# Kernel optimization log

Hardware: AMD Instinct MI355X
Metric: run time of the kernel (lower is better)

Reference implementation:

```python
import jax, jax.numpy as jnp
import numpy as np

B, N, D, H = 32, 4096, 768, 384

def setup_inputs() -> dict:
    key = jax.random.key(0)
    k1, k2, k3 = jax.random.split(key, 3)
    patch_tokens = jax.random.normal(k1, (B, N, D), dtype=jnp.float32)
    # score head params (kaiming-like scale)
    w1 = jax.random.normal(k2, (D, H), dtype=jnp.float32) * (2.0 / H) ** 0.5
    b1 = jnp.zeros((H,), dtype=jnp.float32)
    w2 = jax.random.normal(k3, (H,), dtype=jnp.float32) * (2.0 / 1) ** 0.5
    b2 = jnp.zeros((), dtype=jnp.float32)
    return {"patch_tokens": patch_tokens, "w1": w1, "b1": b1, "w2": w2, "b2": b2,
            "keep_ratio_pct": 50}

def reference(patch_tokens, w1, b1, w2, b2, keep_ratio_pct):
    # score head: Linear -> GELU (erf variant, torch default) -> Linear(->1)
    h = jax.nn.gelu(jnp.einsum('bnd,dh->bnh', patch_tokens, w1) + b1, approximate=False)
    patch_logits = jnp.einsum('bnh,h->bn', h, w2) + b2                 # [B, N]
    foreground_scores = jax.nn.sigmoid(patch_logits)                    # [B, N]

    patch_count = patch_tokens.shape[1]
    keep_count = max(1, int(patch_count * keep_ratio_pct / 100))
    keep_count = min(keep_count, patch_count)

    if keep_count == patch_count:
        keep_mask = jnp.ones_like(foreground_scores)
    else:
        topk_scores, _ = jax.lax.top_k(foreground_scores, keep_count)   # [B, k], sorted desc
        keep_threshold = jax.lax.stop_gradient(topk_scores[:, -1:])     # [B, 1]
        keep_mask = (foreground_scores >= keep_threshold).astype(foreground_scores.dtype)

    filtered_scores = foreground_scores * keep_mask
    filtered_weights = filtered_scores / (jnp.sum(filtered_scores, axis=1, keepdims=True) + 1e-12)
    filtered_feat = jnp.einsum('bn,bnd->bd', filtered_weights, patch_tokens)  # [B, D]
    return (filtered_feat, filtered_weights, foreground_scores, keep_mask)
```

## Files before the change

kernel.cpp:

```cpp
#include <hip/hip_runtime.h>
#include <math.h>

#define BB 32
#define NN 4096
#define DD 768
#define HH 384
#define NCH 8

typedef _Float16 half8 __attribute__((ext_vector_type(8)));
typedef float f32x4 __attribute__((ext_vector_type(4)));

__global__ __launch_bounds__(64) void fapf_prep_w(
    const float* __restrict__ w1, short* __restrict__ whf, short* __restrict__ wlf)
{
    const int cf = blockIdx.x;
    const int kg = blockIdx.y;
    const int l  = threadIdx.x;
    const int c  = cf * 16 + (l & 15);
    const int kb = kg * 32 + (l >> 4) * 8;

    short hs[8], ls[8];
#pragma unroll
    for (int i = 0; i < 8; i++) {
        float v = w1[(size_t)(kb + i) * HH + c];
        _Float16 hi = (_Float16)v;
        _Float16 lo = (_Float16)(v - (float)hi);
        hs[i] = *(short*)&hi;
        ls[i] = *(short*)&lo;
    }
    size_t base = ((size_t)(kg * 24 + cf) * 64 + l) * 8;
#pragma unroll
    for (int i = 0; i < 8; i++) { whf[base + i] = hs[i]; wlf[base + i] = ls[i]; }
}

__global__ __launch_bounds__(256)
__attribute__((amdgpu_waves_per_eu(3)))
void fapf_scores_mfma(
    const float* __restrict__ x, const short* __restrict__ whf,
    const short* __restrict__ wlf, const float* __restrict__ b1,
    const float* __restrict__ w2, const float* __restrict__ b2,
    float* __restrict__ scores)
{
    __shared__ __align__(16) short xh[2][32 * 64];
    __shared__ __align__(16) short xl[2][32 * 64];
    __shared__ float part[32][4];

    const int tid = threadIdx.x;
    const int l   = tid & 63;
    const int cw  = tid >> 6;
    const int t0  = blockIdx.x * 32;

    f32x4 acc[2][6];
#pragma unroll
    for (int fr = 0; fr < 2; fr++)
#pragma unroll
        for (int cf = 0; cf < 6; cf++) acc[fr][cf] = (f32x4){0.f, 0.f, 0.f, 0.f};

    const half8* whp = (const half8*)whf + (size_t)(cw * 6) * 64 + l;
    const half8* wlp = (const half8*)wlf + (size_t)(cw * 6) * 64 + l;

    float4 xv[2];

#define LOADX(ch)                                                            \
    {                                                                        \
        _Pragma("unroll")                                                    \
        for (int it = 0; it < 2; it++) {                                     \
            int id = it * 256 + tid;                                         \
            xv[it] = *(const float4*)&x[(size_t)(t0 + (id >> 4)) * DD        \
                                        + (ch) * 64 + (id & 15) * 4];        \
        }                                                                    \
    }

#define SPLITWRITE(buf)                                                      \
    {                                                                        \
        _Pragma("unroll")                                                    \
        for (int it = 0; it < 2; it++) {                                     \
            int id = it * 256 + tid;                                         \
            int row = id >> 4, seg = id & 15;                                \
            union { short s[4]; uint2 u; } ph, pl;                           \
            float vv[4] = {xv[it].x, xv[it].y, xv[it].z, xv[it].w};          \
            _Pragma("unroll")                                                \
            for (int i = 0; i < 4; i++) {                                    \
                _Float16 hi = (_Float16)vv[i];                               \
                _Float16 lo = (_Float16)(vv[i] - (float)hi);                 \
                ph.s[i] = *(short*)&hi;                                      \
                pl.s[i] = *(short*)&lo;                                      \
            }                                                                \
            int idx = (row * 64 + seg * 4) ^ ((row & 7) << 3);               \
            *(uint2*)&xh[buf][idx] = ph.u;                                   \
            *(uint2*)&xl[buf][idx] = pl.u;                                   \
        }                                                                    \
    }

#define LOADB(dst, ptr, kg)                                                  \
    {                                                                        \
        _Pragma("unroll")                                                    \
        for (int cf = 0; cf < 6; cf++)                                       \
            dst[cf] = (ptr)[(size_t)(kg) * 1536 + (size_t)cf * 64];          \
    }

    LOADX(0);
    SPLITWRITE(0);
    half8 bA[6], bB[6];
    LOADB(bA, whp, 0);
    __syncthreads();
    LOADX(1);

    for (int c = 0; c < 12; c++) {
        const int cur = c & 1;

#pragma unroll
        for (int ks = 0; ks < 2; ks++) {
            const int kg = c * 2 + ks;

            half8 ah[2], al[2];
#pragma unroll
            for (int fr = 0; fr < 2; fr++) {
                int row = fr * 16 + (l & 15);
                int idx = (row * 64 + ks * 32 + (l >> 4) * 8) ^ ((row & 7) << 3);
                ah[fr] = *(const half8*)&xh[cur][idx];
                al[fr] = *(const half8*)&xl[cur][idx];
            }

            LOADB(bB, wlp, kg);

            __builtin_amdgcn_s_setprio(1);
#pragma unroll
            for (int fr = 0; fr < 2; fr++)
#pragma unroll
                for (int cf = 0; cf < 6; cf++)
                    acc[fr][cf] = __builtin_amdgcn_mfma_f32_16x16x32_f16(
                        ah[fr], bA[cf], acc[fr][cf], 0, 0, 0);
#pragma unroll
            for (int fr = 0; fr < 2; fr++)
#pragma unroll
                for (int cf = 0; cf < 6; cf++)
                    acc[fr][cf] = __builtin_amdgcn_mfma_f32_16x16x32_f16(
                        al[fr], bA[cf], acc[fr][cf], 0, 0, 0);
            __builtin_amdgcn_s_setprio(0);

            if (kg < 23) LOADB(bA, whp, kg + 1);

            __builtin_amdgcn_s_setprio(1);
#pragma unroll
            for (int fr = 0; fr < 2; fr++)
#pragma unroll
                for (int cf = 0; cf < 6; cf++)
                    acc[fr][cf] = __builtin_amdgcn_mfma_f32_16x16x32_f16(
                        ah[fr], bB[cf], acc[fr][cf], 0, 0, 0);
            __builtin_amdgcn_s_setprio(0);
        }

        if (c < 11) {
            SPLITWRITE(cur ^ 1);
            __syncthreads();
            if (c < 10) LOADX(c + 2);
        }
    }

    float b1v[6], w2v[6];
#pragma unroll
    for (int cf = 0; cf < 6; cf++) {
        int col = cw * 96 + cf * 16 + (l & 15);
        b1v[cf] = b1[col];
        w2v[cf] = w2[col];
    }
    float p[2][4];
#pragma unroll
    for (int fr = 0; fr < 2; fr++)
#pragma unroll
        for (int j = 0; j < 4; j++) p[fr][j] = 0.f;
#pragma unroll
    for (int fr = 0; fr < 2; fr++)
#pragma unroll
        for (int cf = 0; cf < 6; cf++)
#pragma unroll
            for (int j = 0; j < 4; j++) {
                float hh = acc[fr][cf][j] + b1v[cf];
                float g  = 0.5f * hh * (1.f + erff(hh * 0.70710678118654752f));
                p[fr][j] = fmaf(g, w2v[cf], p[fr][j]);
            }
#pragma unroll
    for (int m = 8; m >= 1; m >>= 1)
#pragma unroll
        for (int fr = 0; fr < 2; fr++)
#pragma unroll
            for (int j = 0; j < 4; j++)
                p[fr][j] += __shfl_xor(p[fr][j], m, 64);

    if ((l & 15) == 0) {
#pragma unroll
        for (int fr = 0; fr < 2; fr++)
#pragma unroll
            for (int j = 0; j < 4; j++) {
                int row = fr * 16 + (l >> 4) * 4 + j;
                part[row][cw] = p[fr][j];
            }
    }
    __syncthreads();
    if (tid < 32) {
        float lg = part[tid][0] + part[tid][1] + part[tid][2] + part[tid][3] + b2[0];
        scores[t0 + tid] = 1.f / (1.f + expf(-lg));
    }
#undef LOADX
#undef SPLITWRITE
#undef LOADB
}

__global__ __launch_bounds__(1024) void fapf_select_kernel(
    const float* __restrict__ scores, const int* __restrict__ pct_p,
    float* __restrict__ weights, float* __restrict__ mask,
    float* __restrict__ feat, int* __restrict__ kidx,
    float* __restrict__ kw, int* __restrict__ kcnt)
{
    __shared__ float s[NN];
    __shared__ float red[1024];
    __shared__ int scnt;
    const int b = blockIdx.x, tid = threadIdx.x;

    if (tid == 0) scnt = 0;
    for (int i = tid; i < DD; i += 1024) feat[b * DD + i] = 0.f;
    for (int i = tid; i < NN; i += 1024) s[i] = scores[b * NN + i];
    __syncthreads();

    for (int k = 2; k <= NN; k <<= 1) {
        for (int j = k >> 1; j > 0; j >>= 1) {
            for (int i = tid; i < NN; i += 1024) {
                int ixj = i ^ j;
                if (ixj > i) {
                    bool up = ((i & k) == 0);
                    float a = s[i], c = s[ixj];
                    if (up ? (a > c) : (a < c)) { s[i] = c; s[ixj] = a; }
                }
            }
            __syncthreads();
        }
    }

    int pct = pct_p[0];
    long long kcl = (long long)NN * pct / 100;
    int kc = (int)kcl;
    if (kc < 1) kc = 1;
    if (kc > NN) kc = NN;
    float thr = s[NN - kc];

    float local = 0.f;
    for (int i = tid; i < NN; i += 1024) {
        float v = scores[b * NN + i];
        if (v >= thr) local += v;
    }
    red[tid] = local;
    __syncthreads();
    for (int step = 512; step > 0; step >>= 1) {
        if (tid < step) red[tid] += red[tid + step];
        __syncthreads();
    }
    float inv = 1.f / (red[0] + 1e-12f);
    const int lane = tid & 63;
    for (int i = tid; i < NN; i += 1024) {
        float v = scores[b * NN + i];
        bool keep = (v >= thr);
        float m = keep ? 1.f : 0.f;
        weights[b * NN + i] = v * m * inv;
        mask[b * NN + i]    = m;
        if (kidx) {
            unsigned long long bal = __ballot(keep);
            int base = 0;
            if (lane == 0) base = atomicAdd(&scnt, __popcll(bal));
            base = __shfl(base, 0, 64);
            if (keep) {
                int off = __popcll(bal & ((1ULL << lane) - 1ULL));
                kidx[b * NN + base + off] = i;
                kw[b * NN + base + off]   = v * inv;
            }
        }
    }
    if (kidx) {
        __syncthreads();
        if (tid == 0) kcnt[b] = scnt;
    }
}

__global__ __launch_bounds__(256) void fapf_feat_compact(
    const float* __restrict__ x, const int* __restrict__ kidx,
    const float* __restrict__ kw, const int* __restrict__ kcnt,
    float* __restrict__ feat)
{
    const int b  = blockIdx.y;
    const int d0 = blockIdx.x * 64;
    const int ch = blockIdx.z;
    const int dl = threadIdx.x & 63;
    const int ng = threadIdx.x >> 6;

    const int cnt = kcnt[b];
    int per = (cnt + NCH - 1) / NCH;
    int j0 = ch * per; if (j0 > cnt) j0 = cnt;
    int j1 = j0 + per; if (j1 > cnt) j1 = cnt;
    int len = j1 - j0;
    int per_w = (len + 3) >> 2;
    int s = j0 + ng * per_w;
    int e = s + per_w; if (e > j1) e = j1;

    const float* xb  = x + (size_t)b * NN * DD + d0 + dl;
    const int*   ib  = kidx + b * NN;
    const float* wbp = kw + b * NN;

    float a[8];
#pragma unroll
    for (int u = 0; u < 8; u++) a[u] = 0.f;

    int j = s;
    for (; j + 8 <= e; j += 8) {
        int   idx[8];
        float ww[8];
#pragma unroll
        for (int u = 0; u < 8; u++) { idx[u] = ib[j + u]; ww[u] = wbp[j + u]; }
#pragma unroll
        for (int u = 0; u < 8; u++)
            a[u] = fmaf(ww[u], xb[(size_t)idx[u] * DD], a[u]);
    }
    for (; j < e; j++)
        a[0] = fmaf(wbp[j], xb[(size_t)ib[j] * DD], a[0]);

    float acc = ((a[0] + a[1]) + (a[2] + a[3])) + ((a[4] + a[5]) + (a[6] + a[7]));

    __shared__ float red[4][64];
    red[ng][dl] = acc;
    __syncthreads();
    if (threadIdx.x < 64) {
        float v = (red[0][dl] + red[1][dl]) + (red[2][dl] + red[3][dl]);
        atomicAdd(&feat[b * DD + d0 + dl], v);
    }
}

__global__ __launch_bounds__(256) void fapf_feat_dense(
    const float* __restrict__ x, const float* __restrict__ weights,
    float* __restrict__ feat)
{
    const int b  = blockIdx.y;
    const int d0 = blockIdx.x * 64;
    const int dl = threadIdx.x & 63;
    const int ng = threadIdx.x >> 6;

    const float* xb = x + (size_t)b * NN * DD;
    const float* wb = weights + b * NN;

    float a0 = 0.f, a1 = 0.f, a2 = 0.f, a3 = 0.f;
    for (int n = ng; n < NN; n += 16) {
        float w0 = wb[n], w1v = wb[n + 4], w2v = wb[n + 8], w3 = wb[n + 12];
        float v0 = xb[(size_t)(n)      * DD + d0 + dl];
        float v1 = xb[(size_t)(n + 4)  * DD + d0 + dl];
        float v2 = xb[(size_t)(n + 8)  * DD + d0 + dl];
        float v3 = xb[(size_t)(n + 12) * DD + d0 + dl];
        a0 = fmaf(w0, v0, a0);
        a1 = fmaf(w1v, v1, a1);
        a2 = fmaf(w2v, v2, a2);
        a3 = fmaf(w3, v3, a3);
    }
    float acc = (a0 + a1) + (a2 + a3);

    __shared__ float red[4][64];
    red[ng][dl] = acc;
    __syncthreads();
    if (threadIdx.x < 64) {
        feat[b * DD + d0 + dl] =
            (red[0][dl] + red[1][dl]) + (red[2][dl] + red[3][dl]);
    }
}

extern "C" void kernel_launch(void* const* d_in, const int* in_sizes, int n_in,
                              void* d_out, int out_size, void* d_ws, size_t ws_size,
                              hipStream_t stream) {
    const float* x   = (const float*)d_in[0];
    const float* w1  = (const float*)d_in[1];
    const float* b1  = (const float*)d_in[2];
    const float* w2  = (const float*)d_in[3];
    const float* b2  = (const float*)d_in[4];
    const int*   pct = (const int*)d_in[5];

    float* out = (float*)d_out;
    float* feat    = out;
    float* weights = out + BB * DD;
    float* scores  = weights + BB * NN;
    float* mask    = scores + BB * NN;

    short* whf  = (short*)d_ws;
    short* wlf  = whf + 24 * 24 * 64 * 8;
    int*   kidx = (int*)(wlf + 24 * 24 * 64 * 8);
    float* kw   = (float*)(kidx + BB * NN);
    int*   kcnt = (int*)(kw + BB * NN);

    const size_t needed = 2 * (size_t)(24 * 24 * 64 * 8) * sizeof(short)
                        + (size_t)BB * NN * (sizeof(int) + sizeof(float))
                        + BB * sizeof(int);
    const bool compact = ws_size >= needed;

    fapf_prep_w<<<dim3(24, 24), dim3(64), 0, stream>>>(w1, whf, wlf);
    fapf_scores_mfma<<<dim3(BB * NN / 32), dim3(256), 0, stream>>>(
        x, whf, wlf, b1, w2, b2, scores);
    fapf_select_kernel<<<dim3(BB), dim3(1024), 0, stream>>>(
        scores, pct, weights, mask, feat,
        compact ? kidx : (int*)nullptr, kw, kcnt);
    if (compact) {
        fapf_feat_compact<<<dim3(DD / 64, BB, NCH), dim3(256), 0, stream>>>(
            x, kidx, kw, kcnt, feat);
    } else {
        fapf_feat_dense<<<dim3(DD / 64, BB), dim3(256), 0, stream>>>(
            x, weights, feat);
    }
}
```

Baseline: 357.6 us.

## Triple-buffer weight fragments with two-step prefetch and packed fp16 split conversion

```diff
diff --git a/kernel.cpp b/kernel.cpp
--- a/kernel.cpp
+++ b/kernel.cpp
@@ -8,6 +8,7 @@
 #define NCH 8
 
 typedef _Float16 half8 __attribute__((ext_vector_type(8)));
+typedef __fp16 fp16x2 __attribute__((ext_vector_type(2)));
 typedef float f32x4 __attribute__((ext_vector_type(4)));
 
 __global__ __launch_bounds__(64) void fapf_prep_w(
@@ -77,18 +78,22 @@
         for (int it = 0; it < 2; it++) {                                     \
             int id = it * 256 + tid;                                         \
             int row = id >> 4, seg = id & 15;                                \
-            union { short s[4]; uint2 u; } ph, pl;                           \
             float vv[4] = {xv[it].x, xv[it].y, xv[it].z, xv[it].w};          \
-            _Pragma("unroll")                                                \
-            for (int i = 0; i < 4; i++) {                                    \
-                _Float16 hi = (_Float16)vv[i];                               \
-                _Float16 lo = (_Float16)(vv[i] - (float)hi);                 \
-                ph.s[i] = *(short*)&hi;                                      \
-                pl.s[i] = *(short*)&lo;                                      \
-            }                                                                \
+            union { fp16x2 h; unsigned int u; float f; } h0, h1, p0, p1;     \
+            h0.h = __builtin_amdgcn_cvt_pkrtz(vv[0], vv[1]);                 \
+            h1.h = __builtin_amdgcn_cvt_pkrtz(vv[2], vv[3]);                 \
+            float l0 = vv[0] - (float)h0.h[0];                               \
+            float l1 = vv[1] - (float)h0.h[1];                               \
+            float l2 = vv[2] - (float)h1.h[0];                               \
+            float l3 = vv[3] - (float)h1.h[1];                               \
+            p0.h = __builtin_amdgcn_cvt_pkrtz(l0, l1);                       \
+            p1.h = __builtin_amdgcn_cvt_pkrtz(l2, l3);                       \
+            uint2 uh, ul;                                                    \
+            uh.x = h0.u; uh.y = h1.u;                                        \
+            ul.x = p0.u; ul.y = p1.u;                                        \
             int idx = (row * 64 + seg * 4) ^ ((row & 7) << 3);               \
-            *(uint2*)&xh[buf][idx] = ph.u;                                   \
-            *(uint2*)&xl[buf][idx] = pl.u;                                   \
+            *(uint2*)&xh[buf][idx] = uh;                                     \
+            *(uint2*)&xl[buf][idx] = ul;                                     \
         }                                                                    \
     }
 
@@ -99,62 +104,75 @@
             dst[cf] = (ptr)[(size_t)(kg) * 1536 + (size_t)cf * 64];          \
     }
 
+    half8 b[3][6];
+    half8 ah[2], al[2];
+
     LOADX(0);
     SPLITWRITE(0);
-    half8 bA[6], bB[6];
-    LOADB(bA, whp, 0);
+    LOADB(b[0], whp, 0);
+    LOADB(b[1], wlp, 0);
     __syncthreads();
     LOADX(1);
 
-    for (int c = 0; c < 12; c++) {
-        const int cur = c & 1;
-
-#pragma unroll
-        for (int ks = 0; ks < 2; ks++) {
-            const int kg = c * 2 + ks;
-
-            half8 ah[2], al[2];
-#pragma unroll
-            for (int fr = 0; fr < 2; fr++) {
-                int row = fr * 16 + (l & 15);
-                int idx = (row * 64 + ks * 32 + (l >> 4) * 8) ^ ((row & 7) << 3);
-                ah[fr] = *(const half8*)&xh[cur][idx];
-                al[fr] = *(const half8*)&xl[cur][idx];
-            }
-
-            LOADB(bB, wlp, kg);
-
-            __builtin_amdgcn_s_setprio(1);
-#pragma unroll
-            for (int fr = 0; fr < 2; fr++)
-#pragma unroll
-                for (int cf = 0; cf < 6; cf++)
-                    acc[fr][cf] = __builtin_amdgcn_mfma_f32_16x16x32_f16(
-                        ah[fr], bA[cf], acc[fr][cf], 0, 0, 0);
-#pragma unroll
-            for (int fr = 0; fr < 2; fr++)
-#pragma unroll
-                for (int cf = 0; cf < 6; cf++)
-                    acc[fr][cf] = __builtin_amdgcn_mfma_f32_16x16x32_f16(
-                        al[fr], bA[cf], acc[fr][cf], 0, 0, 0);
-            __builtin_amdgcn_s_setprio(0);
-
-            if (kg < 23) LOADB(bA, whp, kg + 1);
-
-            __builtin_amdgcn_s_setprio(1);
-#pragma unroll
-            for (int fr = 0; fr < 2; fr++)
-#pragma unroll
-                for (int cf = 0; cf < 6; cf++)
-                    acc[fr][cf] = __builtin_amdgcn_mfma_f32_16x16x32_f16(
-                        ah[fr], bB[cf], acc[fr][cf], 0, 0, 0);
-            __builtin_amdgcn_s_setprio(0);
-        }
-
-        if (c < 11) {
-            SPLITWRITE(cur ^ 1);
-            __syncthreads();
-            if (c < 10) LOADX(c + 2);
+    for (int sc = 0; sc < 4; sc++) {
+#pragma unroll
+        for (int cc = 0; cc < 3; cc++) {
+            const int c   = sc * 3 + cc;
+            const int cur = c & 1;
+#pragma unroll
+            for (int tp = 0; tp < 4; tp++) {
+                const int tloc  = cc * 4 + tp;
+                const int u     = tloc % 3;
+                const int ui    = (tloc + 2) % 3;
+                const int kind  = tp & 1;
+                const int ks    = tp >> 1;
+                const int kindi = (tloc + 2) & 1;
+
+                int kgi = (sc * 12 + tloc + 2) >> 1;
+                if (kgi > 23) kgi = 23;
+                if (kindi == 0) { LOADB(b[ui], whp, kgi); }
+                else            { LOADB(b[ui], wlp, kgi); }
+
+                if (kind == 0) {
+#pragma unroll
+                    for (int fr = 0; fr < 2; fr++) {
+                        int row = fr * 16 + (l & 15);
+                        int idx = (row * 64 + ks * 32 + (l >> 4) * 8)
+                                  ^ ((row & 7) << 3);
+                        ah[fr] = *(const half8*)&xh[cur][idx];
+                        al[fr] = *(const half8*)&xl[cur][idx];
+                    }
+                    __builtin_amdgcn_s_setprio(1);
+#pragma unroll
+                    for (int fr = 0; fr < 2; fr++)
+#pragma unroll
+                        for (int cf = 0; cf < 6; cf++)
+                            acc[fr][cf] = __builtin_amdgcn_mfma_f32_16x16x32_f16(
+                                ah[fr], b[u][cf], acc[fr][cf], 0, 0, 0);
+#pragma unroll
+                    for (int fr = 0; fr < 2; fr++)
+#pragma unroll
+                        for (int cf = 0; cf < 6; cf++)
+                            acc[fr][cf] = __builtin_amdgcn_mfma_f32_16x16x32_f16(
+                                al[fr], b[u][cf], acc[fr][cf], 0, 0, 0);
+                    __builtin_amdgcn_s_setprio(0);
+                } else {
+                    __builtin_amdgcn_s_setprio(1);
+#pragma unroll
+                    for (int fr = 0; fr < 2; fr++)
+#pragma unroll
+                        for (int cf = 0; cf < 6; cf++)
+                            acc[fr][cf] = __builtin_amdgcn_mfma_f32_16x16x32_f16(
+                                ah[fr], b[u][cf], acc[fr][cf], 0, 0, 0);
+                    __builtin_amdgcn_s_setprio(0);
+                }
+            }
+
+            if (c < 11) {
+                SPLITWRITE(cur ^ 1);
+                __syncthreads();
+                if (c < 10) LOADX(c + 2);
+            }
         }
     }
 
```

Measured after the change: 542.0 us. 1.52x slower.
